# Optimization experiments

Hardware: AMD Instinct MI355X
Metric: run time of the kernel (lower is better)

## Reference

```python
import jax, jax.numpy as jnp
import numpy as np
from jax import lax

# ---- quantum-kernel constants: flipped model f = Tr[rho(theta) O(patch)] ----
# rho(theta) = (I + sum_i theta_i P_i)/4 over the 15 non-identity 2-qubit Paulis.
# O(patch)  = (M + M^T)/2 where M is the 3x3 patch zero-padded to 16 and reshaped 4x4.
# Both are linear in their inputs, so precompute A[i,k] = Re Tr[P_i O(e_k)] and
# t0[k] = Tr[O(e_k)] once on the host.

def _pauli_features():
    I = np.eye(2, dtype=np.complex64)
    X = np.array([[0, 1], [1, 0]], np.complex64)
    Y = np.array([[0, -1j], [1j, 0]], np.complex64)
    Z = np.array([[1, 0], [0, -1]], np.complex64)
    singles = [I, X, Y, Z]
    paulis = [np.kron(a, b) for a in singles for b in singles][1:]  # 15 non-identity
    A = np.zeros((15, 9), np.float32)
    t0 = np.zeros((9,), np.float32)
    for k in range(9):
        M = np.zeros((4, 4), np.complex64)
        M.flat[k] = 1.0
        O = (M + M.conj().T) / 2.0
        t0[k] = float(np.real(np.trace(O)))
        for i, P in enumerate(paulis):
            A[i, k] = float(np.real(np.trace(P @ O)))
    return A, t0

_A_NP, _T0_NP = _pauli_features()
STRIDE = 1
PAD = (1, 1)  # (pad_h, pad_w)


def setup_inputs() -> dict:
    key = jax.random.key(0)
    k1, k2, k3 = jax.random.split(key, 3)
    x = jax.random.normal(k1, (32, 16, 128, 128), dtype=jnp.float32)
    weight = jax.random.normal(k2, (64, 16, 15), dtype=jnp.float32)
    bias = jax.random.normal(k3, (64, 1), dtype=jnp.float32)
    return {"x": x, "weight": weight, "bias": bias}


def reference(x, weight, bias):
    B, C, H, W = x.shape
    ph, pw = PAD
    Ho = (H - 3 + 2 * ph) // STRIDE + 1
    Wo = (W - 3 + 2 * pw) // STRIDE + 1
    # im2col: [B, C*9, Ho, Wo], channel-major (C slowest, 3x3 row-major fastest)
    patches = lax.conv_general_dilated_patches(
        x, (3, 3), (STRIDE, STRIDE), ((ph, ph), (pw, pw)))
    patches = patches.reshape(B, C, 9, Ho * Wo)  # [B, C, 9, P]

    A = jnp.asarray(_A_NP)    # [15, 9]
    t0 = jnp.asarray(_T0_NP)  # [9]

    # identity part of rho: sum over in-channels of Tr[O]/4 (weight-independent)
    base = jnp.einsum('k,bckp->bp', t0, patches)            # [B, P]
    # Pauli features Tr[P_i O(patch)] per (channel, patch)
    qf = jnp.einsum('ik,bckp->bcip', A, patches)            # [B, C, 15, P]
    out = (base[:, None, :] + jnp.einsum('oci,bcip->bop', weight, qf)) * 0.25
    out = out + bias                                        # bias [O,1] -> [B,O,P]
    return out.reshape(B, weight.shape[0], Ho, Wo)
```

## Files before the change

### kernel.cpp

```cpp
#include <hip/hip_runtime.h>
#include <hip/hip_bf16.h>


typedef short bf16x8 __attribute__((ext_vector_type(8)));
typedef float f32x4 __attribute__((ext_vector_type(4)));

__device__ __forceinline__ void pauli_entry(int s, int r, int c, float& re, float& im) {
    re = 0.f; im = 0.f;
    if (s == 0)      { if (r == c) re = 1.f; }
    else if (s == 1) { if (r != c) re = 1.f; }
    else if (s == 2) { if (r == 0 && c == 1) im = -1.f; else if (r == 1 && c == 0) im = 1.f; }
    else             { if (r == c) re = (r == 0) ? 1.f : -1.f; }
}

__device__ __forceinline__ float A_entry(int i, int k) {
    int j = i + 1, sa = j >> 2, sb = j & 3;
    int r = k >> 2, c = k & 3;
    float ar, ai, br, bi;
    pauli_entry(sa, r >> 1, c >> 1, ar, ai);
    pauli_entry(sb, r & 1, c & 1, br, bi);
    float re1 = ar * br - ai * bi;
    pauli_entry(sa, c >> 1, r >> 1, ar, ai);
    pauli_entry(sb, c & 1, r & 1, br, bi);
    float re2 = ar * br - ai * bi;
    return 0.5f * (re1 + re2);
}

__device__ __forceinline__ short f2bf(float f) {
    union { float f; unsigned int u; } a; a.f = f;
    unsigned int r = a.u + 0x7fffu + ((a.u >> 16) & 1u);
    return (short)(r >> 16);
}

__device__ __forceinline__ unsigned pk_bf16(float a, float b) {
#if __has_builtin(__builtin_amdgcn_cvt_pk_bf16_f32)
    typedef __bf16 bf2 __attribute__((ext_vector_type(2)));
    bf2 r = __builtin_amdgcn_cvt_pk_bf16_f32(a, b);
    union { bf2 v; unsigned u; } cv; cv.v = r;
    return cv.u;
#else
    union { float f; unsigned u; } x, y; x.f = a; y.f = b;
    unsigned ra = x.u + 0x7fffu + ((x.u >> 16) & 1u);
    unsigned rb = y.u + 0x7fffu + ((y.u >> 16) & 1u);
    return (ra >> 16) | (rb & 0xffff0000u);
#endif
}

__global__ __launch_bounds__(256) void prep_kernel(const float* __restrict__ weight,
                                                   short* __restrict__ bfrag) {
    __shared__ float Ash[135];
    int tid = threadIdx.x;
    if (tid < 135) Ash[tid] = A_entry(tid / 9, tid % 9);
    __syncthreads();

    int t = blockIdx.x * 256 + tid;
    if (t >= 1280) return;
    int lane  = t & 63;
    int ot    = (t >> 6) & 3;
    int chunk = t >> 8;
    int q     = lane >> 4;
    int o     = ot * 16 + (lane & 15);
    short vals[8];
    #pragma unroll
    for (int j = 0; j < 8; ++j) {
        int gk = chunk * 32 + q * 8 + j;
        float v = 0.f;
        if (gk < 144) {
            int tap = gk >> 4;
            int c   = gk & 15;
            float acc = (tap == 0 || tap == 5) ? 1.f : 0.f;
            const float* w = weight + (o * 16 + c) * 15;
            #pragma unroll
            for (int i = 0; i < 15; ++i) acc += w[i] * Ash[i * 9 + tap];
            v = 0.25f * acc;
        }
        vals[j] = f2bf(v);
    }
    *(bf16x8*)(bfrag + t * 8) = *(bf16x8*)vals;
}

__global__ __launch_bounds__(256, 4) void conv_mfma(const float* __restrict__ x,
                                                    const short* __restrict__ bfrag,
                                                    const float* __restrict__ bias,
                                                    float* __restrict__ out) {
    __shared__ short sx[6 * 136 * 16];

    const int tid  = threadIdx.x;
    const int h0   = blockIdx.x * 4;
    const int b    = blockIdx.y;
    const int lane = tid & 63;
    const int wave = tid >> 6;
    const int q    = lane >> 4;
    const int nlo  = lane & 15;
    const int otp  = wave >> 1;
    const int rh   = wave & 1;

    const float* xb = x + (size_t)b * 16 * 128 * 128;
    #pragma unroll
    for (int it = 0; it < 7; ++it) {
        int pos = tid + it * 256;
        if (pos < 1632) {
            int seg = pos / 136;
            int w   = pos - seg * 136;
            int row = seg >> 1, chalf = seg & 1;
            int hp  = h0 - 1 + row;
            int xw  = w - 4;
            bool ok = ((unsigned)hp < 128u) && ((unsigned)xw < 128u);
            const float* src = xb + (size_t)(chalf * 8) * 16384 + hp * 128 + xw;
            float v[8];
            #pragma unroll
            for (int j = 0; j < 8; ++j)
                v[j] = ok ? src[(size_t)j * 16384] : 0.f;
            int slot = (chalf ^ (w >> 2)) & 1;
            unsigned* dst = (unsigned*)sx + (row * 136 + w) * 8 + slot * 4;
            #pragma unroll
            for (int j2 = 0; j2 < 4; ++j2)
                dst[j2] = pk_bf16(v[2 * j2], v[2 * j2 + 1]);
        }
    }

    bf16x8 Breg[10];
    #pragma unroll
    for (int ch = 0; ch < 5; ++ch)
        #pragma unroll
        for (int j = 0; j < 2; ++j)
            Breg[ch * 2 + j] = *(const bf16x8*)(bfrag + ((ch * 4 + otp * 2 + j) * 64 + lane) * 8);
    float bv[2];
    #pragma unroll
    for (int j = 0; j < 2; ++j) bv[j] = bias[(otp * 2 + j) * 16 + nlo];

    int baseA[5];
    #pragma unroll
    for (int ch = 0; ch < 5; ++ch) {
        int tap = ch * 2 + (q >> 1);
        if (tap > 8) tap = 8;
        int kh = tap / 3, kw = tap - 3 * kh;
        int chalf = q & 1;
        int row0  = rh * 2 + kh;
        int w0    = nlo + kw + 3;
        int slot  = (chalf ^ (w0 >> 2)) & 1;
        baseA[ch] = (row0 * 136 + w0) * 16 + slot * 8;
    }
    __syncthreads();

    #pragma unroll
    for (int r = 0; r < 2; ++r) {
        const int h = h0 + rh * 2 + r;
        #pragma unroll
        for (int np = 0; np < 4; ++np) {
            f32x4 acc[2][2];
            #pragma unroll
            for (int j = 0; j < 2; ++j) {
                f32x4 ini = { bv[j], bv[j], bv[j], bv[j] };
                acc[j][0] = ini;
                acc[j][1] = ini;
            }
            #pragma unroll
            for (int ch = 0; ch < 5; ++ch) {
                const short* pA = sx + baseA[ch] + r * 2176 + np * 512;
                bf16x8 A0 = *(const bf16x8*)(pA);
                bf16x8 A1 = *(const bf16x8*)(pA + 256);
                #pragma unroll
                for (int j = 0; j < 2; ++j) {
                    acc[j][0] = __builtin_amdgcn_mfma_f32_16x16x32_bf16(A0, Breg[ch * 2 + j], acc[j][0], 0, 0, 0);
                    acc[j][1] = __builtin_amdgcn_mfma_f32_16x16x32_bf16(A1, Breg[ch * 2 + j], acc[j][1], 0, 0, 0);
                }
            }
            #pragma unroll
            for (int j = 0; j < 2; ++j) {
                float* dst = out + (((size_t)b * 64 + (otp * 2 + j) * 16 + nlo) * 128 + h) * 128
                           + np * 32 + q * 4;
                *(f32x4*)dst        = acc[j][0];
                *(f32x4*)(dst + 16) = acc[j][1];
            }
        }
    }
}

extern "C" void kernel_launch(void* const* d_in, const int* in_sizes, int n_in,
                              void* d_out, int out_size, void* d_ws, size_t ws_size,
                              hipStream_t stream) {
    const float* x      = (const float*)d_in[0];
    const float* weight = (const float*)d_in[1];
    const float* bias   = (const float*)d_in[2];
    float* out   = (float*)d_out;
    short* bfrag = (short*)d_ws;

    prep_kernel<<<5, 256, 0, stream>>>(weight, bfrag);
    dim3 grid(32, 32);
    conv_mfma<<<grid, 256, 0, stream>>>(x, bfrag, bias, out);
}
```

Baseline: 166.9 us.

## Pre-convert input to padded bf16 layout and stage via global_load_lds

Adds a separate pass that converts x to a zero-padded, channel-interleaved, swizzled bf16 buffer in workspace. The conv kernel then fills its shared-memory tile with direct global-to-LDS 16-byte loads instead of strided fp32 loads and in-kernel conversion. This removes the redundant halo reloading and conversion work from the conv kernel. In exchange it adds an extra kernel launch and a full write plus reread of a bf16 copy of the input. It also reads somewhat beyond the 6 needed rows, since 7*256*8 shorts is 14336.

Measured after the change: 175.2 us. 1.05x slower.

```diff
diff --git a/kernel.cpp b/kernel.cpp
--- a/kernel.cpp
+++ b/kernel.cpp
@@ -4,6 +4,7 @@
 
 typedef short bf16x8 __attribute__((ext_vector_type(8)));
 typedef float f32x4 __attribute__((ext_vector_type(4)));
+typedef unsigned u32x4 __attribute__((ext_vector_type(4)));
 
 __device__ __forceinline__ void pauli_entry(int s, int r, int c, float& re, float& im) {
     re = 0.f; im = 0.f;
@@ -46,6 +47,12 @@
 #endif
 }
 
+__device__ __forceinline__ void gload_lds16(const short* g, short* l) {
+    __builtin_amdgcn_global_load_lds(
+        (const __attribute__((address_space(1))) unsigned*)g,
+        (__attribute__((address_space(3))) unsigned*)l, 16, 0, 0);
+}
+
 __global__ __launch_bounds__(256) void prep_kernel(const float* __restrict__ weight,
                                                    short* __restrict__ bfrag) {
     __shared__ float Ash[135];
@@ -79,11 +86,39 @@
     *(bf16x8*)(bfrag + t * 8) = *(bf16x8*)vals;
 }
 
-__global__ __launch_bounds__(256, 4) void conv_mfma(const float* __restrict__ x,
+__global__ __launch_bounds__(256) void convert_kernel(const float* __restrict__ x,
+                                                      short* __restrict__ xs) {
+    int task = blockIdx.x * 256 + threadIdx.x;
+    if (task >= 130 * 136) return;
+    int hp = task / 136;
+    int wp = task - hp * 136;
+    int b  = blockIdx.y;
+    int h  = hp - 1;
+    int xw = wp - 4;
+    bool ok = ((unsigned)h < 128u) && ((unsigned)xw < 128u);
+
+    const float* src = x + ((size_t)b * 16) * 16384 + h * 128 + xw;
+    float v[16];
+    #pragma unroll
+    for (int c = 0; c < 16; ++c)
+        v[c] = ok ? src[(size_t)c * 16384] : 0.f;
+
+    u32x4 A, B;
+    #pragma unroll
+    for (int p = 0; p < 4; ++p) {
+        A[p] = pk_bf16(v[2 * p],     v[2 * p + 1]);
+        B[p] = pk_bf16(v[8 + 2 * p], v[8 + 2 * p + 1]);
+    }
+    unsigned* dst = (unsigned*)(xs + ((size_t)b * 131 + hp) * 2176 + wp * 16);
+    if (((wp >> 2) & 1) == 0) { *(u32x4*)dst = A; *(u32x4*)(dst + 4) = B; }
+    else                      { *(u32x4*)dst = B; *(u32x4*)(dst + 4) = A; }
+}
+
+__global__ __launch_bounds__(256, 4) void conv_mfma(const short* __restrict__ xs,
                                                     const short* __restrict__ bfrag,
                                                     const float* __restrict__ bias,
                                                     float* __restrict__ out) {
-    __shared__ short sx[6 * 136 * 16];
+    __shared__ short sx[14336];
 
     const int tid  = threadIdx.x;
     const int h0   = blockIdx.x * 4;
@@ -95,28 +130,11 @@
     const int otp  = wave >> 1;
     const int rh   = wave & 1;
 
-    const float* xb = x + (size_t)b * 16 * 128 * 128;
+    const short* xsb = xs + ((size_t)b * 131 + h0) * 2176;
     #pragma unroll
     for (int it = 0; it < 7; ++it) {
-        int pos = tid + it * 256;
-        if (pos < 1632) {
-            int seg = pos / 136;
-            int w   = pos - seg * 136;
-            int row = seg >> 1, chalf = seg & 1;
-            int hp  = h0 - 1 + row;
-            int xw  = w - 4;
-            bool ok = ((unsigned)hp < 128u) && ((unsigned)xw < 128u);
-            const float* src = xb + (size_t)(chalf * 8) * 16384 + hp * 128 + xw;
-            float v[8];
-            #pragma unroll
-            for (int j = 0; j < 8; ++j)
-                v[j] = ok ? src[(size_t)j * 16384] : 0.f;
-            int slot = (chalf ^ (w >> 2)) & 1;
-            unsigned* dst = (unsigned*)sx + (row * 136 + w) * 8 + slot * 4;
-            #pragma unroll
-            for (int j2 = 0; j2 < 4; ++j2)
-                dst[j2] = pk_bf16(v[2 * j2], v[2 * j2 + 1]);
-        }
+        int u = tid + it * 256;
+        gload_lds16(xsb + (size_t)u * 8, sx + (size_t)u * 8);
     }
 
     bf16x8 Breg[10];
@@ -185,8 +203,11 @@
     const float* bias   = (const float*)d_in[2];
     float* out   = (float*)d_out;
     short* bfrag = (short*)d_ws;
+    short* xs    = (short*)((char*)d_ws + 32768);
 
     prep_kernel<<<5, 256, 0, stream>>>(weight, bfrag);
+    dim3 cgrid((130 * 136 + 255) / 256, 32);
+    convert_kernel<<<cgrid, 256, 0, stream>>>(x, xs);
     dim3 grid(32, 32);
-    conv_mfma<<<grid, 256, 0, stream>>>(x, bfrag, bias, out);
-}
+    conv_mfma<<<grid, 256, 0, stream>>>(xs, bfrag, bias, out);
+}
```
